# Performance work log

Hardware: AMD Instinct MI355X
Metric: run time of the kernel (lower is better)

The kernel has to match this reference:

```python
import jax, jax.numpy as jnp
import numpy as np

B, T, HID = 2, 1024, 1024
NQ, NK, DK, DV = 8, 4, 128, 128
KDIM, KKDIM, KVDIM, VDIM = NQ * DK, NK * DK, NK * DV, NQ * DV  # 1024, 512, 512, 1024
CONV_DIM = KDIM + KKDIM + KVDIM  # 2048
KSZ = 4
EPS = 1e-5


def setup_inputs() -> dict:
    ks = jax.random.split(jax.random.key(0), 6)
    tot = KDIM + KKDIM + KVDIM + VDIM + NQ + NQ  # 3104
    return {
        "x": jax.random.normal(ks[0], (B, T, HID), jnp.float32),
        "w_in": jax.random.normal(ks[1], (HID, tot), jnp.float32) * 0.02,
        "conv_w": jax.random.normal(ks[2], (CONV_DIM, KSZ), jnp.float32) * 0.3,
        "A_log": jax.random.uniform(ks[3], (NQ,), jnp.float32, 0.0, 1.0),
        "dt_bias": jnp.ones((NQ,), jnp.float32),
        "norm_w": jnp.ones((DV,), jnp.float32),
        "w_out": jax.random.normal(ks[4], (VDIM, HID), jnp.float32) * 0.02,
    }


def _l2norm(u):
    return u * jax.lax.rsqrt(jnp.sum(u * u, axis=-1, keepdims=True) + 1e-6)


def _forward(x, w_in, conv_w, A_log, dt_bias, norm_w, w_out):
    # merged input projection -> q | k | v | z(gate) | b(beta) | a(decay)
    mixed = x @ w_in  # [B,T,3104]
    o1, o2, o3, o4, o5 = KDIM, KDIM + KKDIM, KDIM + KKDIM + KVDIM, KDIM + KKDIM + KVDIM + VDIM, KDIM + KKDIM + KVDIM + VDIM + NQ
    q, k, v, z, b, a = jnp.split(mixed, [o1, o2, o3, o4, o5], axis=-1)

    # short causal depthwise conv over concatenated q,k,v + silu
    qkv = jnp.concatenate([q, k, v], axis=-1)  # [B,T,CONV_DIM]
    pad = jnp.pad(qkv, ((0, 0), (KSZ - 1, 0), (0, 0)))
    conv = sum(pad[:, j:j + T, :] * conv_w[:, j] for j in range(KSZ))
    qkv = jax.nn.silu(conv)
    q, k, v = jnp.split(qkv, [KDIM, KDIM + KKDIM], axis=-1)

    q = q.reshape(B, T, NQ, DK)
    k = k.reshape(B, T, NK, DK)
    v = v.reshape(B, T, NK, DV)
    # GQA: repeat kv heads to q heads (kv_proj_rank is None -> plain repeat)
    rep = NQ // NK
    k = jnp.repeat(k, rep, axis=2)
    v = jnp.repeat(v, rep, axis=2)

    # qk l2-norm in kernel + query scaling
    q = _l2norm(q) * (DK ** -0.5)
    k = _l2norm(k)

    beta = jax.nn.sigmoid(b)                                # [B,T,NQ]
    g = -jnp.exp(A_log) * jax.nn.softplus(a + dt_bias)      # [B,T,NQ] log-decay

    tm = lambda u: jnp.moveaxis(u, 1, 0)  # time-major for scan

    def step(S, inp):
        # S: [B,NQ,DK,DV]
        qt, kt, vt, gt, bt = inp
        S = S * jnp.exp(gt)[..., None, None]
        vt = bt[..., None] * (vt - jnp.einsum('bhk,bhkv->bhv', kt, S))
        S = S + kt[..., None] * vt[..., None, :]
        ot = jnp.einsum('bhk,bhkv->bhv', qt, S)
        return S, ot

    S0 = jnp.zeros((B, NQ, DK, DV), x.dtype)
    _, o = jax.lax.scan(step, S0, (tm(q), tm(k), tm(v), tm(g), tm(beta)))
    o = jnp.moveaxis(o, 0, 1)  # [B,T,NQ,DV]

    # gated RMS norm with z, then output projection
    zz = z.reshape(B, T, NQ, DV)
    o = o * jax.lax.rsqrt(jnp.mean(o * o, axis=-1, keepdims=True) + EPS)
    o = o * norm_w * jax.nn.silu(zz)
    return o.reshape(B, T, VDIM) @ w_out


def reference(x, w_in, conv_w, A_log, dt_bias, norm_w, w_out):
    return _forward(x, w_in, conv_w, A_log, dt_bias, norm_w, w_out)
```

## Files before the change

kernel.cpp:

```cpp
#include <hip/hip_runtime.h>
#include <hip/hip_bf16.h>
#include <math.h>

#define BB    2
#define TT    1024
#define HID   1024
#define NQ    8
#define NK    4
#define DK    128
#define DV    128
#define TOT   3088
#define CONVD 2048
#define KSZ   4
#define BT    (BB*TT)
#define CHUNK 64
#define NCHUNK (TT/CHUNK)
#define NBH   (BB*NQ)
#define NPAD1 3200

typedef __attribute__((ext_vector_type(8))) short short8v;
typedef __attribute__((ext_vector_type(4))) float f32x4;
typedef unsigned short ushort_t;
typedef unsigned int uint_t;

__device__ __forceinline__ float siluf(float x)     { return x / (1.f + expf(-x)); }
__device__ __forceinline__ float sigmoidf_(float x) { return 1.f / (1.f + expf(-x)); }
__device__ __forceinline__ float softplusf_(float x){ return x > 15.f ? x : log1pf(expf(x)); }

__device__ __forceinline__ ushort_t f2bf(float f) {
    uint_t u = __builtin_bit_cast(uint_t, f);
    u = (u + 0x7fff + ((u >> 16) & 1)) >> 16;
    return (ushort_t)u;
}
__device__ __forceinline__ float bf2f(ushort_t u) {
    uint_t v = ((uint_t)u) << 16;
    return __builtin_bit_cast(float, v);
}
__device__ __forceinline__ ushort4 pack4(f32x4 v) {
    ushort4 p; p.x = f2bf(v[0]); p.y = f2bf(v[1]); p.z = f2bf(v[2]); p.w = f2bf(v[3]);
    return p;
}

__global__ __launch_bounds__(256) void f2bf_kernel(const float* __restrict__ src,
                                                   ushort_t* __restrict__ dst) {
    int i = (blockIdx.x * 256 + threadIdx.x) * 4;
    float4 v = *(const float4*)(src + i);
    ushort4 o;
    o.x = f2bf(v.x); o.y = f2bf(v.y); o.z = f2bf(v.z); o.w = f2bf(v.w);
    *(ushort4*)(dst + i) = o;
}

__global__ __launch_bounds__(256) void transpose_f2bf(const float* __restrict__ src,
                                                      ushort_t* __restrict__ dst,
                                                      int K, int N) {
    __shared__ float tile[32][33];
    int n0 = blockIdx.x * 32, k0 = blockIdx.y * 32;
    int c = threadIdx.x & 31, rbase = threadIdx.x >> 5;
    #pragma unroll
    for (int i = 0; i < 4; i++) {
        int r = rbase + i * 8;
        int n = n0 + c;
        tile[r][c] = (n < N) ? src[(size_t)(k0 + r) * N + n] : 0.f;
    }
    __syncthreads();
    #pragma unroll
    for (int i = 0; i < 4; i++) {
        int r = rbase + i * 8;
        dst[(size_t)(n0 + r) * K + k0 + c] = f2bf(tile[c][r]);
    }
}

__global__ __launch_bounds__(256) void gemm_bf16(const ushort_t* __restrict__ A,
                                                 const ushort_t* __restrict__ BTm,
                                                 float* __restrict__ C,
                                                 int K, int Nc, int ldc) {
    __shared__ ushort_t As[128 * 32];
    __shared__ ushort_t Bs[128 * 32];
    int tid = threadIdx.x;
    int wave = tid >> 6, lane = tid & 63;
    int wr = wave >> 1, wc = wave & 1;
    int row0 = blockIdx.y * 128, col0 = blockIdx.x * 128;

    f32x4 zero4 = {0.f, 0.f, 0.f, 0.f};
    f32x4 acc[4][4];
    #pragma unroll
    for (int m = 0; m < 4; m++)
        #pragma unroll
        for (int n = 0; n < 4; n++) acc[m][n] = zero4;

    int srow = wave * 32 + (lane >> 2);
    int koff = (lane & 3) * 8;
    const ushort_t* gA0 = A + (size_t)(row0 + srow) * K + koff;
    const ushort_t* gA1 = A + (size_t)(row0 + srow + 16) * K + koff;
    const ushort_t* gB0 = BTm + (size_t)(col0 + srow) * K + koff;
    const ushort_t* gB1 = BTm + (size_t)(col0 + srow + 16) * K + koff;
    ushort_t* lA0 = As + (wave * 2 + 0) * 512;
    ushort_t* lA1 = As + (wave * 2 + 1) * 512;
    ushort_t* lB0 = Bs + (wave * 2 + 0) * 512;
    ushort_t* lB1 = Bs + (wave * 2 + 1) * 512;

    for (int k0 = 0; k0 < K; k0 += 32) {
        __builtin_amdgcn_global_load_lds(
            (const __attribute__((address_space(1))) void*)(gA0 + k0),
            (__attribute__((address_space(3))) void*)lA0, 16, 0, 0);
        __builtin_amdgcn_global_load_lds(
            (const __attribute__((address_space(1))) void*)(gA1 + k0),
            (__attribute__((address_space(3))) void*)lA1, 16, 0, 0);
        __builtin_amdgcn_global_load_lds(
            (const __attribute__((address_space(1))) void*)(gB0 + k0),
            (__attribute__((address_space(3))) void*)lB0, 16, 0, 0);
        __builtin_amdgcn_global_load_lds(
            (const __attribute__((address_space(1))) void*)(gB1 + k0),
            (__attribute__((address_space(3))) void*)lB1, 16, 0, 0);
        __syncthreads();

        short8v af[4], bf[4];
        #pragma unroll
        for (int m = 0; m < 4; m++)
            af[m] = *(const short8v*)(As + (wr * 64 + m * 16 + (lane & 15)) * 32 + (lane >> 4) * 8);
        #pragma unroll
        for (int n = 0; n < 4; n++)
            bf[n] = *(const short8v*)(Bs + (wc * 64 + n * 16 + (lane & 15)) * 32 + (lane >> 4) * 8);
        #pragma unroll
        for (int m = 0; m < 4; m++)
            #pragma unroll
            for (int n = 0; n < 4; n++)
                acc[m][n] = __builtin_amdgcn_mfma_f32_16x16x32_bf16(af[m], bf[n], acc[m][n], 0, 0, 0);
        __syncthreads();
    }

    #pragma unroll
    for (int m = 0; m < 4; m++) {
        #pragma unroll
        for (int n = 0; n < 4; n++) {
            int row = row0 + wr * 64 + m * 16 + (lane >> 4) * 4;
            int col = col0 + wc * 64 + n * 16 + (lane & 15);
            if (col < Nc) {
                #pragma unroll
                for (int e = 0; e < 4; e++)
                    C[(size_t)(row + e) * ldc + col] = acc[m][n][e];
            }
        }
    }
}

__global__ __launch_bounds__(256) void conv_split_kernel(const float* __restrict__ mixed,
                                                         const float* __restrict__ conv_w,
                                                         const float* __restrict__ A_log,
                                                         const float* __restrict__ dt_bias,
                                                         ushort_t* __restrict__ qb,
                                                         ushort_t* __restrict__ kb,
                                                         float* __restrict__ kn,
                                                         float* __restrict__ vn,
                                                         float* __restrict__ beta,
                                                         float* __restrict__ g) {
    int bt = blockIdx.x;
    int t = bt & (TT - 1);
    int tid = threadIdx.x;
    int c0 = tid * 8;

    float val[8];
    #pragma unroll
    for (int i = 0; i < 8; i++) val[i] = 0.f;
    #pragma unroll
    for (int j = 0; j < KSZ; j++) {
        int tt = t - (KSZ - 1) + j;
        if (tt >= 0) {
            const float* src = mixed + (size_t)(bt - (KSZ - 1) + j) * TOT + c0;
            #pragma unroll
            for (int i = 0; i < 8; i++) val[i] += src[i] * conv_w[(c0 + i) * KSZ + j];
        }
    }
    #pragma unroll
    for (int i = 0; i < 8; i++) val[i] = siluf(val[i]);

    float ss = 0.f;
    #pragma unroll
    for (int i = 0; i < 8; i++) ss += val[i] * val[i];
    #pragma unroll
    for (int m = 1; m < 16; m <<= 1) ss += __shfl_xor(ss, m, 64);
    float rs = rsqrtf(ss + 1e-6f);

    if (tid < 128) {
        float sc = rs * 0.08838834764831845f;
        short8v pk;
        #pragma unroll
        for (int i = 0; i < 8; i++) pk[i] = (short)f2bf(val[i] * sc);
        *(short8v*)(qb + (size_t)bt * 1024 + c0) = pk;
    } else if (tid < 192) {
        int o = c0 - 1024;
        short8v pk;
        #pragma unroll
        for (int i = 0; i < 8; i++) {
            float kv = val[i] * rs;
            kn[(size_t)bt * 512 + o + i] = kv;
            pk[i] = (short)f2bf(kv);
        }
        *(short8v*)(kb + (size_t)bt * 512 + o) = pk;
    } else {
        #pragma unroll
        for (int i = 0; i < 8; i++) vn[(size_t)bt * 512 + (c0 - 1536) + i] = val[i];
    }
    if (tid < 8) {
        beta[bt * 8 + tid] = sigmoidf_(mixed[(size_t)bt * TOT + 3072 + tid]);
    } else if (tid < 16) {
        int h = tid - 8;
        g[bt * 8 + h] = -expf(A_log[h]) * softplusf_(mixed[(size_t)bt * TOT + 3080 + h] + dt_bias[h]);
    }
}

__global__ __launch_bounds__(256) void phaseA_kernel(const float* __restrict__ kn,
                                                     const float* __restrict__ vn,
                                                     const float* __restrict__ beta,
                                                     const float* __restrict__ g,
                                                     float* __restrict__ W,
                                                     ushort_t* __restrict__ Znegb,
                                                     ushort_t* __restrict__ knT,
                                                     float* __restrict__ Bvec) {
    int chunk = blockIdx.x;
    int bh = chunk >> 4, c = chunk & 15;
    int b = bh >> 3, h = bh & 7, hk = h >> 1;
    int bt0 = b * TT + c * CHUNK;
    int tid = threadIdx.x;
    int wave = tid >> 6, lane = tid & 63;
    int lr = lane & 15, lg = lane >> 4;

    __shared__ __align__(16) ushort_t kcb[64 * 128];
    __shared__ float Ms[64][65];
    __shared__ float Bv[64], Bev[64], bev[64];

    if (tid < 64) {
        float v = g[(size_t)(bt0 + tid) * 8 + h];
        #pragma unroll
        for (int off = 1; off < 64; off <<= 1) {
            float n = __shfl_up(v, off, 64);
            if (tid >= off) v += n;
        }
        Bv[tid] = v;
        Bev[tid] = expf(v);
        bev[tid] = beta[(size_t)(bt0 + tid) * 8 + h];
        Bvec[chunk * 64 + tid] = v;
    }
    for (int i = tid; i < 1024; i += 256) {
        int r = i >> 4, k16 = i & 15;
        const float* src = kn + (size_t)(bt0 + r) * 512 + hk * 128 + k16 * 8;
        float4 v0 = *(const float4*)src;
        float4 v1 = *(const float4*)(src + 4);
        short8v pk;
        pk[0] = (short)f2bf(v0.x); pk[1] = (short)f2bf(v0.y);
        pk[2] = (short)f2bf(v0.z); pk[3] = (short)f2bf(v0.w);
        pk[4] = (short)f2bf(v1.x); pk[5] = (short)f2bf(v1.y);
        pk[6] = (short)f2bf(v1.z); pk[7] = (short)f2bf(v1.w);
        int a = (r * 256 + k16 * 16) ^ ((r & 7) << 4);
        *(short8v*)((char*)kcb + a) = pk;
    }
    __syncthreads();

    {
        int t_lane = wave * 16 + lr;
        short8v af[4];
        #pragma unroll
        for (int ks = 0; ks < 4; ks++) {
            int a = (t_lane * 256 + ks * 64 + lg * 16) ^ ((t_lane & 7) << 4);
            af[ks] = *(const short8v*)((const char*)kcb + a);
        }
        for (int sb = 0; sb <= wave; sb++) {
            f32x4 macc = {0.f, 0.f, 0.f, 0.f};
            int s_lane = sb * 16 + lr;
            #pragma unroll
            for (int ks = 0; ks < 4; ks++) {
                int a = (s_lane * 256 + ks * 64 + lg * 16) ^ ((s_lane & 7) << 4);
                short8v bfr = *(const short8v*)((const char*)kcb + a);
                macc = __builtin_amdgcn_mfma_f32_16x16x32_bf16(af[ks], bfr, macc, 0, 0, 0);
            }
            #pragma unroll
            for (int e = 0; e < 4; e++) {
                int trow = wave * 16 + lg * 4 + e;
                int scol = sb * 16 + lr;
                Ms[trow][scol] = (scol < trow) ? macc[e] * bev[trow] * expf(Bv[trow] - Bv[scol]) : 0.f;
            }
        }
    }

    float Xr[64];
    if (tid < 128) {
        #pragma unroll
        for (int t = 0; t < 64; t++)
            Xr[t] = bev[t] * vn[(size_t)(bt0 + t) * 512 + hk * 128 + tid];
    } else {
        int r = tid - 128;
        #pragma unroll
        for (int t = 0; t < 64; t++)
            Xr[t] = bev[t] * Bev[t] * kn[(size_t)(bt0 + t) * 512 + hk * 128 + r];
    }
    __syncthreads();

    #pragma unroll
    for (int t = 1; t < 64; t++) {
        float a0 = 0.f, a1 = 0.f, a2 = 0.f, a3 = 0.f;
        #pragma unroll
        for (int s = 0; s + 4 <= t; s += 4) {
            a0 += Ms[t][s] * Xr[s];     a1 += Ms[t][s + 1] * Xr[s + 1];
            a2 += Ms[t][s + 2] * Xr[s + 2]; a3 += Ms[t][s + 3] * Xr[s + 3];
        }
        #pragma unroll
        for (int s = t & ~3; s < t; s++) a0 += Ms[t][s] * Xr[s];
        Xr[t] -= (a0 + a1) + (a2 + a3);
    }

    if (tid < 128) {
        float* Wc = W + (size_t)chunk * 8192 + tid;
        #pragma unroll
        for (int t = 0; t < 64; t++) Wc[t * 128] = Xr[t];
    } else {
        ushort_t* Zc = Znegb + (size_t)chunk * 8192 + (tid - 128);
        #pragma unroll
        for (int t = 0; t < 64; t++) Zc[t * 128] = f2bf(-Xr[t]);
    }

    if ((h & 1) == 0) {
        ushort_t* kT = knT + (size_t)(b * 4 + hk) * 131072 + c * 64;
        for (int i = tid; i < 8192; i += 256) {
            int r = i >> 6, tt = i & 63;
            int a = (tt * 256 + r * 2) ^ ((tt & 7) << 4);
            kT[(size_t)r * 1024 + tt] = *(const ushort_t*)((const char*)kcb + a);
        }
    }
}

__device__ __forceinline__ int swzSt(int j, int k) {
    int a = j * 256 + k * 2;
    return a ^ ((j & 7) << 4);
}
__device__ __forceinline__ int swzUt(int j, int s) {
    int a = j * 128 + s * 2;
    return a ^ ((j & 7) << 4);
}

__global__ __launch_bounds__(64, 1) void phaseB_mfma(const ushort_t* __restrict__ knT,
                                                     const ushort_t* __restrict__ Znegb,
                                                     const float* __restrict__ W,
                                                     const float* __restrict__ Bvec,
                                                     ushort_t* __restrict__ SallT,
                                                     ushort_t* __restrict__ UTg) {
    int bh = blockIdx.x >> 3, cg = blockIdx.x & 7;
    int b = bh >> 3, h = bh & 7, hk = h >> 1;
    int j0 = cg * 16;
    int lane = threadIdx.x;
    int lr = lane & 15, lg = lane >> 4;

    __shared__ __align__(16) ushort_t St[16 * 128];
    __shared__ __align__(16) ushort_t Ut[16 * 64];

    for (int i = lane * 8; i < 16 * 128; i += 512)
        *(int4*)(St + i) = make_int4(0, 0, 0, 0);

    f32x4 Sacc[8];
    #pragma unroll
    for (int rb = 0; rb < 8; rb++) Sacc[rb] = (f32x4){0.f, 0.f, 0.f, 0.f};

    const ushort_t* kTbase = knT + (size_t)(b * 4 + hk) * 131072;
    int chunk0 = bh * 16;

    for (int c = 0; c < NCHUNK; c++) {
        int chunk = chunk0 + c;
        short8v za[4][4];
        const ushort_t* Zc = Znegb + (size_t)chunk * 8192;
        #pragma unroll
        for (int tb = 0; tb < 4; tb++)
            #pragma unroll
            for (int ks = 0; ks < 4; ks++)
                za[tb][ks] = *(const short8v*)(Zc + (size_t)(tb * 16 + lr) * 128 + ks * 32 + lg * 8);
        short8v ka[8][2];
        #pragma unroll
        for (int rb = 0; rb < 8; rb++)
            #pragma unroll
            for (int ss = 0; ss < 2; ss++)
                ka[rb][ss] = *(const short8v*)(kTbase +
                    (size_t)(rb * 16 + lr) * 1024 + c * 64 + ss * 32 + lg * 8);
        f32x4 wv[4];
        const float* Wc = W + (size_t)chunk * 8192 + j0;
        #pragma unroll
        for (int tb = 0; tb < 4; tb++)
            #pragma unroll
            for (int e = 0; e < 4; e++)
                wv[tb][e] = Wc[(size_t)(tb * 16 + lg * 4 + e) * 128 + lr];
        f32x4 bvw[4];
        #pragma unroll
        for (int tb = 0; tb < 4; tb++)
            bvw[tb] = *(const f32x4*)(Bvec + chunk * 64 + tb * 16 + lg * 4);
        float b63 = Bvec[chunk * 64 + 63];

        ushort_t* SgT = SallT + (size_t)chunk * 16384 + (size_t)(j0 + lr) * 128;
        #pragma unroll
        for (int rb = 0; rb < 8; rb++)
            *(ushort4*)(SgT + rb * 16 + lg * 4) = pack4(Sacc[rb]);

        f32x4 Uacc[4];
        #pragma unroll
        for (int tb = 0; tb < 4; tb++) Uacc[tb] = wv[tb];
        #pragma unroll
        for (int ks = 0; ks < 4; ks++) {
            short8v sb = *(const short8v*)((const char*)St + swzSt(lr, ks * 32 + lg * 8));
            #pragma unroll
            for (int tb = 0; tb < 4; tb++)
                Uacc[tb] = __builtin_amdgcn_mfma_f32_16x16x32_bf16(za[tb][ks], sb, Uacc[tb], 0, 0, 0);
        }

        ushort_t* UTc = UTg + (size_t)chunk * 8192 + (size_t)(j0 + lr) * 64;
        #pragma unroll
        for (int tb = 0; tb < 4; tb++) {
            *(ushort4*)(UTc + tb * 16 + lg * 4) = pack4(Uacc[tb]);
            f32x4 us;
            #pragma unroll
            for (int e = 0; e < 4; e++) us[e] = Uacc[tb][e] * expf(b63 - bvw[tb][e]);
            *(ushort4*)((char*)Ut + swzUt(lr, tb * 16 + lg * 4)) = pack4(us);
        }

        float gC = expf(b63);
        #pragma unroll
        for (int rb = 0; rb < 8; rb++)
            #pragma unroll
            for (int e = 0; e < 4; e++) Sacc[rb][e] *= gC;

        #pragma unroll
        for (int ss = 0; ss < 2; ss++) {
            short8v ub = *(const short8v*)((const char*)Ut + swzUt(lr, ss * 32 + lg * 8));
            #pragma unroll
            for (int rb = 0; rb < 8; rb++)
                Sacc[rb] = __builtin_amdgcn_mfma_f32_16x16x32_bf16(ka[rb][ss], ub, Sacc[rb], 0, 0, 0);
        }

        #pragma unroll
        for (int rb = 0; rb < 8; rb++)
            *(ushort4*)((char*)St + swzSt(lr, rb * 16 + lg * 4)) = pack4(Sacc[rb]);
    }
}

__global__ __launch_bounds__(256) void phaseC_mfma(const ushort_t* __restrict__ qb,
                                                   const ushort_t* __restrict__ kb,
                                                   const ushort_t* __restrict__ UTg,
                                                   const ushort_t* __restrict__ SallT,
                                                   const float* __restrict__ Bvec,
                                                   float* __restrict__ o) {
    int chunk = blockIdx.x;
    int bh = chunk >> 4, c = chunk & 15;
    int b = bh >> 3, h = bh & 7, hk = h >> 1;
    int bt0 = b * TT + c * CHUNK;
    int tid = threadIdx.x, wave = tid >> 6, lane = tid & 63;
    int lr = lane & 15, lg = lane >> 4;

    __shared__ float Bv[64], Bev[64];
    __shared__ __align__(16) ushort_t Pb[64 * 64];

    if (tid < 64) { float v = Bvec[chunk * 64 + tid]; Bv[tid] = v; Bev[tid] = expf(v); }
    __syncthreads();

    int t_lane = wave * 16 + lr;
    const ushort_t* qrow = qb + (size_t)(bt0 + t_lane) * 1024 + h * 128;
    short8v qa[4];
    #pragma unroll
    for (int ks = 0; ks < 4; ks++) qa[ks] = *(const short8v*)(qrow + ks * 32 + lg * 8);

    #pragma unroll
    for (int sb = 0; sb < 4; sb++) {
        f32x4 pacc = {0.f, 0.f, 0.f, 0.f};
        const ushort_t* krow = kb + (size_t)(bt0 + sb * 16 + lr) * 512 + hk * 128;
        #pragma unroll
        for (int ks = 0; ks < 4; ks++) {
            short8v kf = *(const short8v*)(krow + ks * 32 + lg * 8);
            pacc = __builtin_amdgcn_mfma_f32_16x16x32_bf16(qa[ks], kf, pacc, 0, 0, 0);
        }
        int scol = sb * 16 + lr;
        #pragma unroll
        for (int e = 0; e < 4; e++) {
            int trow = wave * 16 + lg * 4 + e;
            float val = (scol <= trow) ? pacc[e] * expf(Bv[trow] - Bv[scol]) : 0.f;
            int a = (trow * 128 + scol * 2) ^ ((trow & 7) << 4);
            *(ushort_t*)((char*)Pb + a) = f2bf(val);
        }
    }

    float Ge[4];
    #pragma unroll
    for (int e = 0; e < 4; e++) Ge[e] = Bev[wave * 16 + lg * 4 + e];
    const ushort_t* ST = SallT + (size_t)chunk * 16384;
    f32x4 acc[8];
    #pragma unroll
    for (int n = 0; n < 8; n++) {
        acc[n] = (f32x4){0.f, 0.f, 0.f, 0.f};
        int j = n * 16 + lr;
        #pragma unroll
        for (int rs = 0; rs < 4; rs++) {
            short8v sf = *(const short8v*)(ST + (size_t)j * 128 + rs * 32 + lg * 8);
            acc[n] = __builtin_amdgcn_mfma_f32_16x16x32_bf16(qa[rs], sf, acc[n], 0, 0, 0);
        }
        #pragma unroll
        for (int e = 0; e < 4; e++) acc[n][e] *= Ge[e];
    }
    __syncthreads();

    short8v pa[2];
    #pragma unroll
    for (int ks = 0; ks < 2; ks++) {
        int a = (t_lane * 128 + (ks * 32 + lg * 8) * 2) ^ ((t_lane & 7) << 4);
        pa[ks] = *(const short8v*)((const char*)Pb + a);
    }
    const ushort_t* UTc = UTg + (size_t)chunk * 8192;
    #pragma unroll
    for (int n = 0; n < 8; n++) {
        int j = n * 16 + lr;
        #pragma unroll
        for (int ks = 0; ks < 2; ks++) {
            short8v uf = *(const short8v*)(UTc + (size_t)j * 64 + ks * 32 + lg * 8);
            acc[n] = __builtin_amdgcn_mfma_f32_16x16x32_bf16(pa[ks], uf, acc[n], 0, 0, 0);
        }
    }
    #pragma unroll
    for (int n = 0; n < 8; n++) {
        int j = n * 16 + lr;
        #pragma unroll
        for (int e = 0; e < 4; e++) {
            int t = wave * 16 + lg * 4 + e;
            o[(size_t)(bt0 + t) * 1024 + h * 128 + j] = acc[n][e];
        }
    }
}

__global__ __launch_bounds__(64) void norm_gate_kernel(const float* __restrict__ o_scan,
                                                       const float* __restrict__ mixed,
                                                       const float* __restrict__ norm_w,
                                                       ushort_t* __restrict__ ginb) {
    int bth = blockIdx.x;
    int bt = bth >> 3, h = bth & 7;
    int lane = threadIdx.x;
    size_t base = (size_t)bt * 1024 + h * 128;
    float o0 = o_scan[base + lane];
    float o1 = o_scan[base + lane + 64];
    float ss = o0 * o0 + o1 * o1;
    #pragma unroll
    for (int m = 1; m < 64; m <<= 1) ss += __shfl_xor(ss, m, 64);
    float r = rsqrtf(ss * (1.f / 128.f) + 1e-5f);
    size_t zbase = (size_t)bt * TOT + 2048 + h * 128;
    float z0 = mixed[zbase + lane];
    float z1 = mixed[zbase + lane + 64];
    ginb[base + lane]      = f2bf(o0 * r * norm_w[lane]      * siluf(z0));
    ginb[base + lane + 64] = f2bf(o1 * r * norm_w[lane + 64] * siluf(z1));
}

extern "C" void kernel_launch(void* const* d_in, const int* in_sizes, int n_in,
                              void* d_out, int out_size, void* d_ws, size_t ws_size,
                              hipStream_t stream) {
    const float* x       = (const float*)d_in[0];
    const float* w_in    = (const float*)d_in[1];
    const float* conv_w  = (const float*)d_in[2];
    const float* A_log   = (const float*)d_in[3];
    const float* dt_bias = (const float*)d_in[4];
    const float* norm_w  = (const float*)d_in[5];
    const float* w_out   = (const float*)d_in[6];
    float* out = (float*)d_out;

    float* ws = (float*)d_ws;
    float* mixed = ws;
    float* kn    = mixed + (size_t)BT * TOT;
    float* vn    = kn + (size_t)BT * 512;
    float* beta  = vn + (size_t)BT * 512;
    float* gdec  = beta + BT * 8;
    float* Wu    = gdec + BT * 8;
    float* Bvec  = Wu + (size_t)BT * 1024;
    float* qbf   = Bvec + NBH * NCHUNK * 64;
    float* kbf   = qbf + 1048576;
    float* knTf  = kbf + 524288;
    float* Znf   = knTf + 524288;
    float* UTf   = Znf + 1048576;
    float* SallTf= UTf + 1048576;
    float* bt2f  = SallTf + 2097152;

    ushort_t* qb    = (ushort_t*)qbf;
    ushort_t* kb    = (ushort_t*)kbf;
    ushort_t* knTb  = (ushort_t*)knTf;
    ushort_t* Znegb = (ushort_t*)Znf;
    ushort_t* UTb   = (ushort_t*)UTf;
    ushort_t* SallT = (ushort_t*)SallTf;
    ushort_t* bt2   = (ushort_t*)bt2f;
    ushort_t* xb    = (ushort_t*)SallTf;
    ushort_t* bt1   = (ushort_t*)knTf;
    ushort_t* ginb  = (ushort_t*)qbf;
    float* oscan    = Wu;

    f2bf_kernel<<<(BT * HID) / 1024, 256, 0, stream>>>(x, xb);
    transpose_f2bf<<<dim3(NPAD1 / 32, HID / 32), 256, 0, stream>>>(w_in, bt1, HID, TOT);
    transpose_f2bf<<<dim3(HID / 32, HID / 32), 256, 0, stream>>>(w_out, bt2, HID, HID);

    gemm_bf16<<<dim3(NPAD1 / 128, BT / 128), 256, 0, stream>>>(xb, bt1, mixed, HID, TOT, TOT);

    conv_split_kernel<<<BT, 256, 0, stream>>>(mixed, conv_w, A_log, dt_bias, qb, kb, kn, vn, beta, gdec);

    phaseA_kernel<<<NBH * NCHUNK, 256, 0, stream>>>(kn, vn, beta, gdec, Wu, Znegb, knTb, Bvec);
    phaseB_mfma<<<NBH * 8, 64, 0, stream>>>(knTb, Znegb, Wu, Bvec, SallT, UTb);
    phaseC_mfma<<<NBH * NCHUNK, 256, 0, stream>>>(qb, kb, UTb, SallT, Bvec, oscan);

    norm_gate_kernel<<<BT * NQ, 64, 0, stream>>>(oscan, mixed, norm_w, ginb);

    gemm_bf16<<<dim3(HID / 128, BT / 128), 256, 0, stream>>>(ginb, bt2, out, HID, HID, HID);
}
```

Measured before the change: 197.3 us.

## Double-buffer phaseB chunk operands in LDS via async global_load_lds prefetch

The sequential chunk recurrence kernel (phaseB) now prefetches the next chunk's Z, kT, W and Bvec tiles into double-buffered, swizzled LDS using global_load_lds. A vmcnt wait gates each chunk on its own loads. The MFMA operands are then read from LDS instead of registers loaded at the top of each iteration. This is meant to hide global memory latency in the serial chunk loop, which runs with only one wave per block. In exchange it adds LDS traffic and relies on a hand-computed vmcnt count and ordering, which is fragile, and there is no barrier, though a single-wave block makes that acceptable.

```diff
diff --git a/kernel.cpp b/kernel.cpp
--- a/kernel.cpp
+++ b/kernel.cpp
@@ -349,6 +349,10 @@
     int lane = threadIdx.x;
     int lr = lane & 15, lg = lane >> 4;
 
+    __shared__ __align__(16) ushort_t Zl[2][64 * 128];
+    __shared__ __align__(16) ushort_t kTl[2][128 * 64];
+    __shared__ __align__(16) float    Wl[2][64 * 16];
+    __shared__ __align__(16) float    Bvl[2][256];
     __shared__ __align__(16) ushort_t St[16 * 128];
     __shared__ __align__(16) ushort_t Ut[16 * 64];
 
@@ -362,34 +366,54 @@
     const ushort_t* kTbase = knT + (size_t)(b * 4 + hk) * 131072;
     int chunk0 = bh * 16;
 
+    auto stage = [&](int chunk, int p) {
+        const char* Zc = (const char*)(Znegb + (size_t)chunk * 8192);
+        #pragma unroll
+        for (int i = 0; i < 16; i++) {
+            int r = 4 * i + (lane >> 4);
+            const char* src = Zc + r * 256 + (((lane & 15) * 16) ^ ((r & 7) << 4));
+            __builtin_amdgcn_global_load_lds(
+                (const __attribute__((address_space(1))) void*)src,
+                (__attribute__((address_space(3))) void*)(&Zl[p][i * 512]), 16, 0, 0);
+        }
+        const char* kc = (const char*)kTbase + (size_t)(chunk & 15) * 128;
+        #pragma unroll
+        for (int i = 0; i < 16; i++) {
+            int r = 8 * i + (lane >> 3);
+            const char* src = kc + (size_t)r * 2048 + (((lane & 7) * 16) ^ ((r & 7) << 4));
+            __builtin_amdgcn_global_load_lds(
+                (const __attribute__((address_space(1))) void*)src,
+                (__attribute__((address_space(3))) void*)(&kTl[p][i * 512]), 16, 0, 0);
+        }
+        const float* Wc = W + (size_t)chunk * 8192 + j0;
+        #pragma unroll
+        for (int i = 0; i < 4; i++) {
+            int r = 16 * i + (lane >> 2);
+            const float* src = Wc + (size_t)r * 128 + (lane & 3) * 4;
+            __builtin_amdgcn_global_load_lds(
+                (const __attribute__((address_space(1))) void*)src,
+                (__attribute__((address_space(3))) void*)(&Wl[p][i * 256]), 16, 0, 0);
+        }
+        const float* bsrc = Bvec + chunk * 64 + (lane & 15) * 4;
+        __builtin_amdgcn_global_load_lds(
+            (const __attribute__((address_space(1))) void*)bsrc,
+            (__attribute__((address_space(3))) void*)(&Bvl[p][0]), 16, 0, 0);
+    };
+
+    stage(chunk0, 0);
+
+    #pragma unroll 1
     for (int c = 0; c < NCHUNK; c++) {
         int chunk = chunk0 + c;
-        short8v za[4][4];
-        const ushort_t* Zc = Znegb + (size_t)chunk * 8192;
-        #pragma unroll
-        for (int tb = 0; tb < 4; tb++)
-            #pragma unroll
-            for (int ks = 0; ks < 4; ks++)
-                za[tb][ks] = *(const short8v*)(Zc + (size_t)(tb * 16 + lr) * 128 + ks * 32 + lg * 8);
-        short8v ka[8][2];
-        #pragma unroll
-        for (int rb = 0; rb < 8; rb++)
-            #pragma unroll
-            for (int ss = 0; ss < 2; ss++)
-                ka[rb][ss] = *(const short8v*)(kTbase +
-                    (size_t)(rb * 16 + lr) * 1024 + c * 64 + ss * 32 + lg * 8);
-        f32x4 wv[4];
-        const float* Wc = W + (size_t)chunk * 8192 + j0;
-        #pragma unroll
-        for (int tb = 0; tb < 4; tb++)
-            #pragma unroll
-            for (int e = 0; e < 4; e++)
-                wv[tb][e] = Wc[(size_t)(tb * 16 + lg * 4 + e) * 128 + lr];
-        f32x4 bvw[4];
-        #pragma unroll
-        for (int tb = 0; tb < 4; tb++)
-            bvw[tb] = *(const f32x4*)(Bvec + chunk * 64 + tb * 16 + lg * 4);
-        float b63 = Bvec[chunk * 64 + 63];
+        int p = c & 1;
+
+        if (c + 1 < NCHUNK) {
+            stage(chunk + 1, p ^ 1);
+            asm volatile("s_waitcnt vmcnt(37)" ::: "memory");
+        } else {
+            asm volatile("s_waitcnt vmcnt(0)" ::: "memory");
+        }
+        __builtin_amdgcn_sched_barrier(0);
 
         ushort_t* SgT = SallT + (size_t)chunk * 16384 + (size_t)(j0 + lr) * 128;
         #pragma unroll
@@ -398,14 +422,26 @@
 
         f32x4 Uacc[4];
         #pragma unroll
-        for (int tb = 0; tb < 4; tb++) Uacc[tb] = wv[tb];
+        for (int tb = 0; tb < 4; tb++)
+            #pragma unroll
+            for (int e = 0; e < 4; e++)
+                Uacc[tb][e] = Wl[p][(tb * 16 + lg * 4 + e) * 16 + lr];
         #pragma unroll
         for (int ks = 0; ks < 4; ks++) {
             short8v sb = *(const short8v*)((const char*)St + swzSt(lr, ks * 32 + lg * 8));
             #pragma unroll
-            for (int tb = 0; tb < 4; tb++)
-                Uacc[tb] = __builtin_amdgcn_mfma_f32_16x16x32_bf16(za[tb][ks], sb, Uacc[tb], 0, 0, 0);
-        }
+            for (int tb = 0; tb < 4; tb++) {
+                int row = tb * 16 + lr;
+                int a = (row * 256 + ks * 64 + lg * 16) ^ ((row & 7) << 4);
+                short8v za = *(const short8v*)((const char*)&Zl[p][0] + a);
+                Uacc[tb] = __builtin_amdgcn_mfma_f32_16x16x32_bf16(za, sb, Uacc[tb], 0, 0, 0);
+            }
+        }
+
+        f32x4 bvw[4];
+        #pragma unroll
+        for (int tb = 0; tb < 4; tb++) bvw[tb] = *(const f32x4*)&Bvl[p][tb * 16 + lg * 4];
+        float b63 = Bvl[p][63];
 
         ushort_t* UTc = UTg + (size_t)chunk * 8192 + (size_t)(j0 + lr) * 64;
         #pragma unroll
@@ -427,8 +463,12 @@
         for (int ss = 0; ss < 2; ss++) {
             short8v ub = *(const short8v*)((const char*)Ut + swzUt(lr, ss * 32 + lg * 8));
             #pragma unroll
-            for (int rb = 0; rb < 8; rb++)
-                Sacc[rb] = __builtin_amdgcn_mfma_f32_16x16x32_bf16(ka[rb][ss], ub, Sacc[rb], 0, 0, 0);
+            for (int rb = 0; rb < 8; rb++) {
+                int row = rb * 16 + lr;
+                int a = (row * 128 + ss * 64 + lg * 16) ^ ((row & 7) << 4);
+                short8v ka = *(const short8v*)((const char*)&kTl[p][0] + a);
+                Sacc[rb] = __builtin_amdgcn_mfma_f32_16x16x32_bf16(ka, ub, Sacc[rb], 0, 0, 0);
+            }
         }
 
         #pragma unroll
```

New measurement: 190.7 us. -3.4%, faster.
